# Kernel tuning notes

Hardware: AMD Instinct MI355X
Metric: run time of the kernel (lower is better)

Reference implementation:

```python
import jax, jax.numpy as jnp
import numpy as np

B, T, D = 2, 2048, 1024
E, K, FF = 8, 2, 4096


def setup_inputs() -> dict:
    key = jax.random.key(0)
    ks = jax.random.split(key, 4)
    scale = 0.02
    return {
        "x": jax.random.normal(ks[0], (B, T, D), jnp.float32),
        "gate_w": jax.random.normal(ks[1], (D, E), jnp.float32) * scale,
        "gate_b": jnp.zeros((E,), jnp.float32),
        "w1": jax.random.normal(ks[2], (E, D, FF), jnp.float32) * scale,
        "b1": jnp.zeros((E, FF), jnp.float32),
        "w2": jax.random.normal(ks[3], (E, FF, D), jnp.float32) * scale,
        "b2": jnp.zeros((E, D), jnp.float32),
    }


def reference(x, gate_w, gate_b, w1, b1, w2, b2):
    # x: (B,T,D). Original runs every expert densely over all tokens then masks;
    # since mask*x == x at selected positions and output is re-masked, the math
    # equals: output[t] = sum_k softmax(topk_vals)[k] * expert_{idx_k}(x)[t].
    n_experts = w1.shape[0]
    gate_logits = x @ gate_w + gate_b                      # (B,T,E)
    topk_vals, topk_idx = jax.lax.top_k(gate_logits, K)    # (B,T,K)
    topk_w = jax.nn.softmax(topk_vals, axis=-1)            # (B,T,K)
    onehot = jax.nn.one_hot(topk_idx, n_experts, dtype=x.dtype)  # (B,T,K,E)
    comb = jnp.sum(onehot * topk_w[..., None], axis=2)     # (B,T,E) combine weights

    # Dense per-expert FFN over all tokens (faithful to original redundant compute)
    h = jax.nn.gelu(jnp.einsum('btd,edf->ebtf', x, w1) + b1[:, None, None, :],
                    approximate=False)                      # (E,B,T,FF)
    y = jnp.einsum('ebtf,efd->ebtd', h, w2) + b2[:, None, None, :]  # (E,B,T,D)
    output = jnp.einsum('ebtd,bte->btd', y, comb)           # (B,T,D)

    expert_counts = jnp.sum(onehot, axis=(0, 1, 2)).astype(jnp.float32)  # (E,)
    return output, gate_logits, topk_idx, expert_counts
```

## Files before the change

### kernel.cpp

```cpp
#include <hip/hip_runtime.h>
#include <math.h>

#define NTOK 4096
#define DIM  1024
#define NE   8
#define FF   4096

#define OUT_LOGITS 4194304
#define OUT_IDX    4227072
#define OUT_CNT    4235264

typedef unsigned short u16;
typedef __bf16 bf16x8 __attribute__((ext_vector_type(8)));
typedef float  f32x4  __attribute__((ext_vector_type(4)));

__device__ __forceinline__ u16 f2bf(float f) {
  union { float f; unsigned u; } v; v.f = f;
  unsigned r = v.u + 0x7fffu + ((v.u >> 16) & 1u);
  return (u16)(r >> 16);
}

__device__ __forceinline__ float gelu_f(float v) {
  float u = v * (0.7978845608f + 0.0356774081f * v * v);
  float e = __expf(2.f * u);
  float t = 1.f - 2.f / (e + 1.f);
  return 0.5f * v * (1.f + t);
}

__device__ __forceinline__ void gload_lds16(const u16* g, u16* l) {
  __builtin_amdgcn_global_load_lds(
      (const __attribute__((address_space(1))) void*)(g),
      (__attribute__((address_space(3))) void*)(l), 16, 0, 0);
}

__global__ __launch_bounds__(256) void transpose_cvt_kernel(const float* __restrict__ in,
                                                            u16* __restrict__ out,
                                                            int R, int C) {
  __shared__ float tile[64][68];
  in  += (size_t)blockIdx.z * R * C;
  out += (size_t)blockIdx.z * R * C;
  int c0 = blockIdx.x * 64, r0 = blockIdx.y * 64;
  int t = threadIdx.x;
  int cr = (t & 15) * 4, rr = t >> 4;
  #pragma unroll
  for (int p = 0; p < 4; p++) {
    float4 v = *(const float4*)(in + (size_t)(r0 + rr + p * 16) * C + c0 + cr);
    *(float4*)&tile[rr + p * 16][cr] = v;
  }
  __syncthreads();
  int c = t >> 2, rb = (t & 3) * 4;
  u16* orow = out + (size_t)(c0 + c) * R + r0;
  #pragma unroll
  for (int it = 0; it < 4; it++) {
    int r = it * 16 + rb;
    ushort4 o;
    o.x = f2bf(tile[r + 0][c]);
    o.y = f2bf(tile[r + 1][c]);
    o.z = f2bf(tile[r + 2][c]);
    o.w = f2bf(tile[r + 3][c]);
    *(ushort4*)(orow + r) = o;
  }
}

__global__ __launch_bounds__(256) void gate_kernel(const float* __restrict__ x,
                                                   const float* __restrict__ gw,
                                                   const float* __restrict__ gb,
                                                   float* __restrict__ out,
                                                   int2* __restrict__ tk_idx,
                                                   float2* __restrict__ tk_w) {
  int wave = threadIdx.x >> 6, lane = threadIdx.x & 63;
  int token = blockIdx.x * 4 + wave;
  const float* xr = x + (size_t)token * DIM + lane * 16;
  float acc[NE];
  #pragma unroll
  for (int e = 0; e < NE; e++) acc[e] = 0.f;
  #pragma unroll
  for (int c = 0; c < 16; c += 4) {
    float4 xv = *(const float4*)(xr + c);
    const float* gwr = gw + (size_t)(lane * 16 + c) * NE;
    float xs[4] = {xv.x, xv.y, xv.z, xv.w};
    #pragma unroll
    for (int q = 0; q < 4; q++)
      #pragma unroll
      for (int e = 0; e < NE; e++)
        acc[e] += xs[q] * gwr[q * NE + e];
  }
  #pragma unroll
  for (int off = 32; off; off >>= 1)
    #pragma unroll
    for (int e = 0; e < NE; e++)
      acc[e] += __shfl_down(acc[e], off);

  if (lane == 0) {
    float lg[NE];
    #pragma unroll
    for (int e = 0; e < NE; e++) {
      lg[e] = acc[e] + gb[e];
      out[OUT_LOGITS + token * NE + e] = lg[e];
    }
    int i0 = 0; float v0 = lg[0];
    #pragma unroll
    for (int e = 1; e < NE; e++) if (lg[e] > v0) { v0 = lg[e]; i0 = e; }
    int i1 = -1; float v1 = -1e30f;
    #pragma unroll
    for (int e = 0; e < NE; e++) if (e != i0 && lg[e] > v1) { v1 = lg[e]; i1 = e; }
    float ex = expf(v1 - v0);
    float s = 1.f + ex;
    out[OUT_IDX + token * 2]     = (float)i0;
    out[OUT_IDX + token * 2 + 1] = (float)i1;
    tk_idx[token] = make_int2(i0, i1);
    tk_w[token]   = make_float2(1.f / s, ex / s);
  }
}

__global__ __launch_bounds__(512) void build_lists_kernel(
    const int2* __restrict__ tk_idx, const float2* __restrict__ tk_w,
    int* __restrict__ counts, int* __restrict__ offsets,
    int* __restrict__ tok_list, float* __restrict__ wt_list,
    float* __restrict__ cnt_out) {
  __shared__ int s_cnt[NE];
  int e = threadIdx.x >> 6, lane = threadIdx.x & 63;
  int cnt = 0;
  for (int base = 0; base < NTOK; base += 64) {
    int2 idx = tk_idx[base + lane];
    cnt += __popcll(__ballot(idx.x == e || idx.y == e));
  }
  if (lane == 0) s_cnt[e] = cnt;
  __syncthreads();
  int off = 0;
  for (int ee = 0; ee < e; ee++) off += s_cnt[ee];
  if (lane == 0) {
    counts[e]  = s_cnt[e];
    offsets[e] = off;
    cnt_out[e] = (float)s_cnt[e];
  }
  int pos = off;
  for (int base = 0; base < NTOK; base += 64) {
    int tok = base + lane;
    int2 idx = tk_idx[tok];
    float2 w = tk_w[tok];
    bool m0 = (idx.x == e), m1 = (idx.y == e);
    bool m = m0 || m1;
    unsigned long long mask = __ballot(m);
    if (m) {
      int p = pos + __popcll(mask & ((1ull << lane) - 1ull));
      tok_list[p] = tok;
      wt_list[p]  = m0 ? w.x : w.y;
    }
    pos += __popcll(mask);
  }
}

__global__ __launch_bounds__(256) void gather_x_kernel(const float* __restrict__ x,
                                                       const int* __restrict__ tok_list,
                                                       u16* __restrict__ xg) {
  int g = blockIdx.x;
  int tok = tok_list[g];
  int c = threadIdx.x * 4;
  float4 v = *(const float4*)(x + (size_t)tok * DIM + c);
  ushort4 o;
  o.x = f2bf(v.x); o.y = f2bf(v.y); o.z = f2bf(v.z); o.w = f2bf(v.w);
  *(ushort4*)(xg + (size_t)g * DIM + c) = o;
}

template <int MODE, int BM, int BN>
__global__ __launch_bounds__(512, 2) void moe_gemm2_kernel(
    const u16* __restrict__ Abase, const u16* __restrict__ Bbase,
    const float* __restrict__ bias,
    const int* __restrict__ counts, const int* __restrict__ offsets,
    const int* __restrict__ tok_list, const float* __restrict__ wt_list,
    u16* __restrict__ Hout, float* __restrict__ Out) {
  constexpr int KT = (MODE == 0) ? DIM : FF;
  constexpr int NT = (MODE == 0) ? FF : DIM;
  constexpr int LA = BM / 64;
  constexpr int LB = BN / 64;
  constexpr int MR = BM / 32;
  constexpr int NR = BN / 64;
  constexpr int ASZ = BM * 64;
  constexpr int BSZ = BN * 64;
  constexpr int NTILES = KT / 64;

  extern __shared__ u16 sm[];

  const int e  = blockIdx.z;
  const int ne = counts[e];
  const int m0 = blockIdx.y * BM;
  if (m0 >= ne) return;
  const int n0   = blockIdx.x * BN;
  const int offs = offsets[e];

  const int t = threadIdx.x;
  const int wave = t >> 6, lane = t & 63;
  const int quad = lane >> 4, l16 = lane & 15;
  const int wmb = (wave & 1) * (BM / 2);
  const int wnb = (wave >> 1) * (BN / 4);

  const u16* aptr[LA];
  const u16* bptr[LB];
  #pragma unroll
  for (int p = 0; p < LA; p++) {
    int idx = p * 512 + t;
    int row = idx >> 3, c = idx & 7;
    int clog = c ^ (row & 7);
    int s = m0 + row; if (s > ne - 1) s = ne - 1;
    aptr[p] = Abase + (size_t)(offs + s) * KT + clog * 8;
  }
  #pragma unroll
  for (int p = 0; p < LB; p++) {
    int idx = p * 512 + t;
    int row = idx >> 3, c = idx & 7;
    int clog = c ^ (row & 7);
    bptr[p] = Bbase + ((size_t)e * NT + n0 + row) * KT + clog * 8;
  }

  auto stage = [&](int buf, int k0) {
    #pragma unroll
    for (int p = 0; p < LA; p++)
      gload_lds16(aptr[p] + k0, sm + buf * ASZ + (p * 512 + t) * 8);
    #pragma unroll
    for (int p = 0; p < LB; p++)
      gload_lds16(bptr[p] + k0, sm + 2 * ASZ + buf * BSZ + (p * 512 + t) * 8);
  };

  const int xrow = l16 & 7;
  const int xo[2] = { ((0 + quad) ^ xrow) * 8, ((4 + quad) ^ xrow) * 8 };
  const int abase0 = (wmb + l16) * 64;
  const int bbase0 = 2 * ASZ + (wnb + l16) * 64;

  f32x4 acc[MR][NR];
  #pragma unroll
  for (int i = 0; i < MR; i++)
    #pragma unroll
    for (int j = 0; j < NR; j++)
      acc[i][j] = (f32x4){0.f, 0.f, 0.f, 0.f};

  stage(0, 0);
  __syncthreads();
  int cur = 0;
  for (int kt = 0; kt < NTILES; ++kt) {
    if (kt + 1 < NTILES) stage(cur ^ 1, (kt + 1) * 64);
    const u16* As = sm + cur * ASZ;
    const u16* Bs = sm + cur * BSZ;
    #pragma unroll
    for (int kk = 0; kk < 2; kk++) {
      bf16x8 a[MR], b[NR];
      #pragma unroll
      for (int i = 0; i < MR; i++) a[i] = *(const bf16x8*)&As[abase0 + i * 1024 + xo[kk]];
      #pragma unroll
      for (int j = 0; j < NR; j++) b[j] = *(const bf16x8*)&Bs[bbase0 + j * 1024 + xo[kk]];
      #pragma unroll
      for (int i = 0; i < MR; i++)
        #pragma unroll
        for (int j = 0; j < NR; j++)
          acc[i][j] = __builtin_amdgcn_mfma_f32_16x16x32_bf16(a[i], b[j], acc[i][j], 0, 0, 0);
    }
    __syncthreads();
    cur ^= 1;
  }

  if (MODE == 0) {
    const float* bb = bias + (size_t)e * FF + n0 + wnb;
    float bc[NR];
    #pragma unroll
    for (int j = 0; j < NR; j++) bc[j] = bb[j * 16 + l16];
    #pragma unroll
    for (int i = 0; i < MR; i++) {
      #pragma unroll
      for (int r = 0; r < 4; r++) {
        int s = m0 + wmb + i * 16 + quad * 4 + r;
        if (s < ne) {
          u16* hr = Hout + (size_t)(offs + s) * FF + n0 + wnb;
          #pragma unroll
          for (int j = 0; j < NR; j++)
            hr[j * 16 + l16] = f2bf(gelu_f(acc[i][j][r] + bc[j]));
        }
      }
    }
  } else {
    const float* bb = bias + (size_t)e * DIM + n0 + wnb;
    float bc[NR];
    #pragma unroll
    for (int j = 0; j < NR; j++) bc[j] = bb[j * 16 + l16];
    #pragma unroll
    for (int i = 0; i < MR; i++) {
      #pragma unroll
      for (int r = 0; r < 4; r++) {
        int s = m0 + wmb + i * 16 + quad * 4 + r;
        if (s < ne) {
          int   tok = tok_list[offs + s];
          float w   = wt_list[offs + s];
          float* orow = Out + (size_t)tok * DIM + n0 + wnb;
          #pragma unroll
          for (int j = 0; j < NR; j++)
            atomicAdd(&orow[j * 16 + l16], (acc[i][j][r] + bc[j]) * w);
        }
      }
    }
  }
}

extern "C" void kernel_launch(void* const* d_in, const int* in_sizes, int n_in,
                              void* d_out, int out_size, void* d_ws, size_t ws_size,
                              hipStream_t stream) {
  const float* x   = (const float*)d_in[0];
  const float* gw  = (const float*)d_in[1];
  const float* gb  = (const float*)d_in[2];
  const float* w1  = (const float*)d_in[3];
  const float* b1  = (const float*)d_in[4];
  const float* w2  = (const float*)d_in[5];
  const float* b2  = (const float*)d_in[6];
  float* out = (float*)d_out;
  char*  ws  = (char*)d_ws;

  u16* w1t = (u16*)(ws);
  u16* w2t = (u16*)(ws + 1ull * 67108864);
  u16* h   = (u16*)(ws + 2ull * 67108864);
  u16* xg  = (u16*)(ws + 3ull * 67108864);
  char* meta = ws + 3ull * 67108864 + 16777216;
  int*    counts   = (int*)(meta);
  int*    offsets  = (int*)(meta + 64);
  int*    tok_list = (int*)(meta + 128);
  float*  wt_list  = (float*)(meta + 128 + 32768);
  int2*   tk_idx   = (int2*)(meta + 128 + 2 * 32768);
  float2* tk_w     = (float2*)(meta + 128 + 2 * 32768 + 32768);
  (void)in_sizes; (void)n_in; (void)out_size; (void)ws_size;

  static bool attr_set = false;
  if (!attr_set) {
    hipFuncSetAttribute(reinterpret_cast<const void*>(moe_gemm2_kernel<0, 256, 256>),
                        hipFuncAttributeMaxDynamicSharedMemorySize, 131072);
    hipFuncSetAttribute(reinterpret_cast<const void*>(moe_gemm2_kernel<1, 128, 256>),
                        hipFuncAttributeMaxDynamicSharedMemorySize, 98304);
    attr_set = true;
  }

  hipMemsetAsync(out, 0, (size_t)OUT_LOGITS * 4, stream);

  transpose_cvt_kernel<<<dim3(FF / 64, DIM / 64, NE), 256, 0, stream>>>(w1, w1t, DIM, FF);
  transpose_cvt_kernel<<<dim3(DIM / 64, FF / 64, NE), 256, 0, stream>>>(w2, w2t, FF, DIM);
  gate_kernel<<<NTOK / 4, 256, 0, stream>>>(x, gw, gb, out, tk_idx, tk_w);
  build_lists_kernel<<<1, 512, 0, stream>>>(tk_idx, tk_w, counts, offsets, tok_list, wt_list,
                                            out + OUT_CNT);
  gather_x_kernel<<<2 * NTOK, 256, 0, stream>>>(x, tok_list, xg);

  moe_gemm2_kernel<0, 256, 256><<<dim3(FF / 256, NTOK / 256, NE), 512, 131072, stream>>>(
      xg, w1t, b1, counts, offsets, tok_list, wt_list, h, nullptr);
  moe_gemm2_kernel<1, 128, 256><<<dim3(DIM / 256, NTOK / 128, NE), 512, 98304, stream>>>(
      h, w2t, b2, counts, offsets, tok_list, wt_list, nullptr, out);
}
```

Before: 620.8 us.

## Split-K the second expert GEMM and fuse weight transposes into one kernel

The two weight transpose-and-convert launches are merged into a single kernel. That kernel uses an XOR-swizzled shared tile and writes 16-byte bf16 vectors. The second GEMM splits its K dimension into two halves across twice as many blocks, and both halves accumulate into the output with atomics, with the bias added only by the first half. This is meant to raise occupancy on the smaller down-projection grid and cut transpose launch and bank-conflict overhead. The cost is twice as many atomic adds to the output.

```diff
diff --git a/kernel.cpp b/kernel.cpp
--- a/kernel.cpp
+++ b/kernel.cpp
@@ -13,6 +13,7 @@
 typedef unsigned short u16;
 typedef __bf16 bf16x8 __attribute__((ext_vector_type(8)));
 typedef float  f32x4  __attribute__((ext_vector_type(4)));
+typedef u16    u16x8  __attribute__((ext_vector_type(8)));
 
 __device__ __forceinline__ u16 f2bf(float f) {
   union { float f; unsigned u; } v; v.f = f;
@@ -33,32 +34,47 @@
       (__attribute__((address_space(3))) void*)(l), 16, 0, 0);
 }
 
-__global__ __launch_bounds__(256) void transpose_cvt_kernel(const float* __restrict__ in,
-                                                            u16* __restrict__ out,
-                                                            int R, int C) {
-  __shared__ float tile[64][68];
-  in  += (size_t)blockIdx.z * R * C;
-  out += (size_t)blockIdx.z * R * C;
-  int c0 = blockIdx.x * 64, r0 = blockIdx.y * 64;
-  int t = threadIdx.x;
-  int cr = (t & 15) * 4, rr = t >> 4;
-  #pragma unroll
-  for (int p = 0; p < 4; p++) {
-    float4 v = *(const float4*)(in + (size_t)(r0 + rr + p * 16) * C + c0 + cr);
-    *(float4*)&tile[rr + p * 16][cr] = v;
+__global__ __launch_bounds__(256) void transpose_cvt2_kernel(
+    const float* __restrict__ w1, u16* __restrict__ w1t,
+    const float* __restrict__ w2, u16* __restrict__ w2t) {
+  __shared__ float tile[4096];
+  int id = blockIdx.x;
+  const float* in; u16* out; int R, C, xt, yt, z;
+  if (id < 8192) {
+    in = w1; out = w1t; R = DIM; C = FF;
+    xt = id & 63; yt = (id >> 6) & 15; z = id >> 10;
+  } else {
+    int i2 = id - 8192;
+    in = w2; out = w2t; R = FF; C = DIM;
+    xt = i2 & 15; yt = (i2 >> 4) & 63; z = i2 >> 10;
+  }
+  in  += (size_t)z * R * C;
+  out += (size_t)z * R * C;
+  const int c0 = xt * 64, r0 = yt * 64;
+  const int t = threadIdx.x;
+
+  {
+    int cc = t & 15, rr = t >> 4;
+    #pragma unroll
+    for (int p = 0; p < 4; p++) {
+      int r = rr + p * 16;
+      float4 v = *(const float4*)(in + (size_t)(r0 + r) * C + c0 + cc * 4);
+      *(float4*)&tile[r * 64 + ((cc ^ (r >> 3)) << 2)] = v;
+    }
   }
   __syncthreads();
-  int c = t >> 2, rb = (t & 3) * 4;
-  u16* orow = out + (size_t)(c0 + c) * R + r0;
-  #pragma unroll
-  for (int it = 0; it < 4; it++) {
-    int r = it * 16 + rb;
-    ushort4 o;
-    o.x = f2bf(tile[r + 0][c]);
-    o.y = f2bf(tile[r + 1][c]);
-    o.z = f2bf(tile[r + 2][c]);
-    o.w = f2bf(tile[r + 3][c]);
-    *(ushort4*)(orow + r) = o;
+  {
+    int h = t & 7, cg = t >> 3;
+    #pragma unroll
+    for (int p = 0; p < 2; p++) {
+      int c = p * 32 + cg;
+      int base = ((((c >> 2) ^ h) << 2)) + (c & 3);
+      u16x8 o;
+      #pragma unroll
+      for (int j = 0; j < 8; j++)
+        o[j] = f2bf(tile[(h * 8 + j) * 64 + base]);
+      *(u16x8*)(out + (size_t)(c0 + c) * R + r0 + h * 8) = o;
+    }
   }
 }
 
@@ -178,11 +194,13 @@
   constexpr int NR = BN / 64;
   constexpr int ASZ = BM * 64;
   constexpr int BSZ = BN * 64;
-  constexpr int NTILES = KT / 64;
+  constexpr int NTILES = (MODE == 0) ? (KT / 64) : (KT / 128);
 
   extern __shared__ u16 sm[];
 
-  const int e  = blockIdx.z;
+  const int zz = blockIdx.z;
+  const int e  = (MODE == 1) ? (zz >> 1) : zz;
+  const int koff = (MODE == 1) ? ((zz & 1) * (KT / 2)) : 0;
   const int ne = counts[e];
   const int m0 = blockIdx.y * BM;
   if (m0 >= ne) return;
@@ -203,14 +221,14 @@
     int row = idx >> 3, c = idx & 7;
     int clog = c ^ (row & 7);
     int s = m0 + row; if (s > ne - 1) s = ne - 1;
-    aptr[p] = Abase + (size_t)(offs + s) * KT + clog * 8;
+    aptr[p] = Abase + (size_t)(offs + s) * KT + koff + clog * 8;
   }
   #pragma unroll
   for (int p = 0; p < LB; p++) {
     int idx = p * 512 + t;
     int row = idx >> 3, c = idx & 7;
     int clog = c ^ (row & 7);
-    bptr[p] = Bbase + ((size_t)e * NT + n0 + row) * KT + clog * 8;
+    bptr[p] = Bbase + ((size_t)e * NT + n0 + row) * KT + koff + clog * 8;
   }
 
   auto stage = [&](int buf, int k0) {
@@ -280,7 +298,7 @@
     const float* bb = bias + (size_t)e * DIM + n0 + wnb;
     float bc[NR];
     #pragma unroll
-    for (int j = 0; j < NR; j++) bc[j] = bb[j * 16 + l16];
+    for (int j = 0; j < NR; j++) bc[j] = (zz & 1) ? 0.f : bb[j * 16 + l16];
     #pragma unroll
     for (int i = 0; i < MR; i++) {
       #pragma unroll
@@ -336,8 +354,7 @@
 
   hipMemsetAsync(out, 0, (size_t)OUT_LOGITS * 4, stream);
 
-  transpose_cvt_kernel<<<dim3(FF / 64, DIM / 64, NE), 256, 0, stream>>>(w1, w1t, DIM, FF);
-  transpose_cvt_kernel<<<dim3(DIM / 64, FF / 64, NE), 256, 0, stream>>>(w2, w2t, FF, DIM);
+  transpose_cvt2_kernel<<<16384, 256, 0, stream>>>(w1, w1t, w2, w2t);
   gate_kernel<<<NTOK / 4, 256, 0, stream>>>(x, gw, gb, out, tk_idx, tk_w);
   build_lists_kernel<<<1, 512, 0, stream>>>(tk_idx, tk_w, counts, offsets, tok_list, wt_list,
                                             out + OUT_CNT);
@@ -345,6 +362,6 @@
 
   moe_gemm2_kernel<0, 256, 256><<<dim3(FF / 256, NTOK / 256, NE), 512, 131072, stream>>>(
       xg, w1t, b1, counts, offsets, tok_list, wt_list, h, nullptr);
-  moe_gemm2_kernel<1, 128, 256><<<dim3(DIM / 256, NTOK / 128, NE), 512, 98304, stream>>>(
+  moe_gemm2_kernel<1, 128, 256><<<dim3(DIM / 256, NTOK / 128, NE * 2), 512, 98304, stream>>>(
       h, w2t, b2, counts, offsets, tok_list, wt_list, nullptr, out);
 }
```

New measurement: 636.3 us. 2.5% more time.
